# Performance work log

Hardware: AMD Instinct MI355X
Metric: run time of the kernel (lower is better)

## Reference

```python
import jax, jax.numpy as jnp
import numpy as np

E, K = 8, 2            # num_experts, top_k
D, H = 1024, 4096      # d_model, expert_hidden_dim
B, S = 4, 2048         # batch, seq
AUX_W = 0.01


def setup_inputs() -> dict:
    key = jax.random.key(0)
    k0, k1, k2, k3 = jax.random.split(key, 4)
    return {
        "x": jax.random.normal(k0, (B, S, D), jnp.float32),
        "router_w": jax.random.normal(k1, (D, E), jnp.float32) * 0.02,  # normal(0.02) init per MoERouter
        "router_b": jnp.zeros((E,), jnp.float32),
        "w_up": jax.random.normal(k2, (E, D, H), jnp.float32) * (1.0 / np.sqrt(D)),
        "b_up": jnp.zeros((E, H), jnp.float32),
        "w_down": jax.random.normal(k3, (E, H, D), jnp.float32) * (1.0 / np.sqrt(H)),
        "b_down": jnp.zeros((E, D), jnp.float32),
    }


def reference(x, router_w, router_b, w_up, b_up, w_down, b_down):
    # Router
    logits = x @ router_w + router_b                       # (B,S,E)
    router_probs = jax.nn.softmax(logits, axis=-1)         # (B,S,E)
    topk_logits, topk_idx = jax.lax.top_k(logits, K)       # (B,S,K)
    topk_p = jax.nn.softmax(topk_logits, axis=-1)          # (B,S,K)

    # Dense all-expert MLP (matches original: every expert computed on every token)
    h = jax.nn.gelu(jnp.einsum('bsd,edh->bseh', x, w_up) + b_up)   # (B,S,E,H)
    all_out = jnp.einsum('bseh,ehd->bsed', h, w_down) + b_down     # (B,S,E,D)

    # Top-k gather + weighted combine
    sel = jnp.take_along_axis(all_out, topk_idx[..., None], axis=2)  # (B,S,K,D)
    output = jnp.sum(topk_p[..., None] * sel, axis=2)                # (B,S,D)

    # Load-balancing aux loss (Switch/Mixtral formulation)
    counts = jnp.zeros((E,), jnp.float32).at[topk_idx.reshape(-1)].add(1.0)
    fraction = counts / (B * S * K)
    prob_mean = router_probs.mean(axis=(0, 1))
    aux_loss = E * jnp.sum(fraction * prob_mean) * AUX_W
    return output, aux_loss, router_probs
```

## Files before the change

kernel.cpp:

```cpp
#include <hip/hip_runtime.h>
#include <hip/hip_bf16.h>
#include <stdint.h>

constexpr int NT = 8192;
constexpr int NE = 8;
constexpr int ND = 1024;
constexpr int NH = 4096;

constexpr int BM = 256;
constexpr int BN = 256;
constexpr int BK = 32;
constexpr int NBUF = 4;
constexpr int KS_DN = 2;

typedef __attribute__((ext_vector_type(8))) short short8;
typedef __attribute__((ext_vector_type(4))) float f32x4;

constexpr size_t O_XBF  = 0;
constexpr size_t O_WUPT = O_XBF  + (size_t)NT * ND * 2;
constexpr size_t O_WDNT = O_WUPT + (size_t)NE * NH * ND * 2;
constexpr size_t O_HBUF = O_WDNT + (size_t)NE * ND * NH * 2;
constexpr size_t O_STOK = O_HBUF + (size_t)NT * 2 * NH * 2;
constexpr size_t O_SP   = O_STOK + (size_t)NT * 2 * 4;
constexpr size_t O_TKE  = O_SP   + (size_t)NT * 2 * 4;
constexpr size_t O_TKP  = O_TKE  + (size_t)NT * 2 * 4;
constexpr size_t O_CTRL = O_TKP  + (size_t)NT * 2 * 4;
constexpr size_t O_TLUP = O_CTRL + 272;
constexpr size_t O_TLDN = O_TLUP + 160 * 4;

__device__ __forceinline__ void gl_lds16(const void* g, void* l) {
  using GP = char __attribute__((address_space(1))) *;
  using LP = char __attribute__((address_space(3))) *;
  __builtin_amdgcn_global_load_lds((GP)(uintptr_t)g, (LP)(uint32_t)(uintptr_t)l, 16, 0, 0);
}

__device__ __forceinline__ float fast_gelu(float x) {
  float u  = 0.7978845608028654f * (x + 0.044715f * x * x * x);
  float ex = __expf(2.0f * u);
  float th = 1.0f - 2.0f / (ex + 1.0f);
  return 0.5f * x * (1.0f + th);
}

__global__ __launch_bounds__(256) void moe_router(
    const float* __restrict__ x, const float* __restrict__ rw, const float* __restrict__ rb,
    __hip_bfloat16* __restrict__ xbf,
    float* __restrict__ probs_out, int* __restrict__ topk_e, float* __restrict__ topk_p,
    int* __restrict__ cnt_ek, float* __restrict__ probsum)
{
  __shared__ float ps[NE];
  __shared__ int cs[16];
  const int tid = threadIdx.x;
  if (tid < NE) ps[tid] = 0.f;
  if (tid < 16) cs[tid] = 0;
  __syncthreads();
  const int lane = tid & 63, wv = tid >> 6;
  for (int it = 0; it < 8; ++it) {
    const int t = blockIdx.x * 4 + wv + it * 1024;
    const float* xr = x + (size_t)t * ND;
    float acc[NE] = {};
#pragma unroll 4
    for (int j = 0; j < 16; ++j) {
      const int d = j * 64 + lane;
      const float xv = xr[d];
      xbf[(size_t)t * ND + d] = __float2bfloat16(xv);
      const float* w = rw + (size_t)d * NE;
#pragma unroll
      for (int ee = 0; ee < NE; ++ee) acc[ee] += xv * w[ee];
    }
#pragma unroll
    for (int ee = 0; ee < NE; ++ee)
#pragma unroll
      for (int off = 32; off >= 1; off >>= 1)
        acc[ee] += __shfl_down(acc[ee], off, 64);
    if (lane == 0) {
      float lg[NE];
#pragma unroll
      for (int ee = 0; ee < NE; ++ee) lg[ee] = acc[ee] + rb[ee];
      float mx = lg[0];
#pragma unroll
      for (int ee = 1; ee < NE; ++ee) mx = fmaxf(mx, lg[ee]);
      float s = 0.f, pe[NE];
#pragma unroll
      for (int ee = 0; ee < NE; ++ee) { pe[ee] = __expf(lg[ee] - mx); s += pe[ee]; }
      const float inv = 1.f / s;
#pragma unroll
      for (int ee = 0; ee < NE; ++ee) {
        const float pr = pe[ee] * inv;
        probs_out[(size_t)t * NE + ee] = pr;
        atomicAdd(&ps[ee], pr);
      }
      int i1 = 0; float l1 = lg[0];
#pragma unroll
      for (int ee = 1; ee < NE; ++ee) if (lg[ee] > l1) { l1 = lg[ee]; i1 = ee; }
      int i2 = 0; float l2 = -3.0e38f;
#pragma unroll
      for (int ee = 0; ee < NE; ++ee) if (ee != i1 && lg[ee] > l2) { l2 = lg[ee]; i2 = ee; }
      const float e2 = __expf(l2 - l1);
      const float dn = 1.f + e2;
      topk_e[t * 2]     = i1;  topk_e[t * 2 + 1] = i2;
      topk_p[t * 2]     = 1.f / dn;
      topk_p[t * 2 + 1] = e2 / dn;
      atomicAdd(&cs[i1 * 2], 1);
      atomicAdd(&cs[i2 * 2 + 1], 1);
    }
  }
  __syncthreads();
  if (tid < NE) atomicAdd(&probsum[tid], ps[tid]);
  if (tid < 16) atomicAdd(&cnt_ek[tid], cs[tid]);
}

__global__ void moe_finalize(const int* __restrict__ cnt_ek, int* __restrict__ off_ek,
                             const float* __restrict__ probsum, float* __restrict__ aux_out,
                             int* __restrict__ ntiles, int* __restrict__ tl_up,
                             int* __restrict__ tl_dn)
{
  __shared__ int c[16], off[16], uoff[8], ucnt[8], doff[16], dcnt[16];
  const int tid = threadIdx.x;
  if (tid < 16) c[tid] = cnt_ek[tid];
  __syncthreads();
  if (tid == 0) {
    int run = 0;
    for (int i = 0; i < 16; ++i) { off[i] = run; run += c[i]; }
    int ur = 0;
    for (int e = 0; e < NE; ++e) {
      ucnt[e] = (c[2 * e] + c[2 * e + 1] + BM - 1) / BM;
      uoff[e] = ur; ur += ucnt[e];
    }
    ntiles[0] = ur;
    int dr = 0;
    for (int i = 0; i < 16; ++i) {
      dcnt[i] = (c[i] + BM - 1) / BM;
      doff[i] = dr; dr += dcnt[i];
    }
    ntiles[1] = dr;
    float aux = 0.f;
    for (int e = 0; e < NE; ++e) {
      float frac = (float)(c[2 * e] + c[2 * e + 1]) / (float)(NT * 2);
      aux += frac * (probsum[e] / (float)NT);
    }
    aux_out[0] = (float)NE * aux * 0.01f;
  }
  __syncthreads();
  if (tid < 16) off_ek[tid] = off[tid];
  if (tid < 8)
    for (int mb = 0; mb < ucnt[tid]; ++mb) tl_up[uoff[tid] + mb] = (tid << 16) | mb;
  if (tid >= 32 && tid < 48) {
    const int i = tid - 32;
    for (int mb = 0; mb < dcnt[i]; ++mb) tl_dn[doff[i] + mb] = (i << 16) | mb;
  }
}

__global__ __launch_bounds__(256) void moe_scatter(
    const int* __restrict__ topk_e, const float* __restrict__ topk_p,
    const int* __restrict__ off_ek, int* __restrict__ fill_ek,
    int* __restrict__ slot_token, float* __restrict__ slot_p)
{
  __shared__ int lc[16], gb[16], offs[16];
  const int tid = threadIdx.x;
  if (tid < 16) lc[tid] = 0;
  __syncthreads();
  const int t = blockIdx.x * 256 + tid;
  const int id0 = topk_e[t * 2] * 2;
  const int id1 = topk_e[t * 2 + 1] * 2 + 1;
  atomicAdd(&lc[id0], 1);
  atomicAdd(&lc[id1], 1);
  __syncthreads();
  if (tid < 16) {
    gb[tid] = atomicAdd(&fill_ek[tid], lc[tid]);
    offs[tid] = off_ek[tid];
    lc[tid] = 0;
  }
  __syncthreads();
  {
    const int r = atomicAdd(&lc[id0], 1);
    const int slot = offs[id0] + gb[id0] + r;
    slot_token[slot] = t;
    slot_p[slot] = topk_p[t * 2];
  }
  {
    const int r = atomicAdd(&lc[id1], 1);
    const int slot = offs[id1] + gb[id1] + r;
    slot_token[slot] = t;
    slot_p[slot] = topk_p[t * 2 + 1];
  }
}

__global__ __launch_bounds__(256) void moe_transpose_cast(
    const float* __restrict__ in, __hip_bfloat16* __restrict__ outp, int Adim, int Bdim)
{
  __shared__ unsigned short tile[64 * 66];
  const int e = blockIdx.z;
  const int b0 = blockIdx.x * 64, a0 = blockIdx.y * 64;
  const float* ip = in + (size_t)e * Adim * Bdim + (size_t)a0 * Bdim + b0;
  const int c4 = (threadIdx.x & 15) * 4;
  const int r0 = threadIdx.x >> 4;
#pragma unroll
  for (int i = 0; i < 4; ++i) {
    const int r = r0 + i * 16;
    const float4 v = *(const float4*)(ip + (size_t)r * Bdim + c4);
    ushort4 u;
    u.x = __hip_bfloat16_raw(__float2bfloat16(v.x)).x;
    u.y = __hip_bfloat16_raw(__float2bfloat16(v.y)).x;
    u.z = __hip_bfloat16_raw(__float2bfloat16(v.z)).x;
    u.w = __hip_bfloat16_raw(__float2bfloat16(v.w)).x;
    *(ushort4*)&tile[r * 66 + c4] = u;
  }
  __syncthreads();
  unsigned short* op = (unsigned short*)outp + (size_t)e * Bdim * Adim + (size_t)b0 * Adim + a0;
  const int cc  = threadIdx.x >> 2;
  const int rr0 = (threadIdx.x & 3) * 16;
  unsigned short u[16];
#pragma unroll
  for (int i = 0; i < 16; ++i) u[i] = tile[(rr0 + i) * 66 + cc];
  *(short8*)(op + (size_t)cc * Adim + rr0)     = *(short8*)&u[0];
  *(short8*)(op + (size_t)cc * Adim + rr0 + 8) = *(short8*)&u[8];
}


__global__ __launch_bounds__(512, 2) void moe_gemm_up(
    const __hip_bfloat16* __restrict__ xbf,
    const __hip_bfloat16* __restrict__ wupT,
    const float* __restrict__ b_up,
    const int* __restrict__ slot_token,
    const int* __restrict__ cnt_ek, const int* __restrict__ off_ek,
    const int* __restrict__ ntiles, const int* __restrict__ tl_up,
    __hip_bfloat16* __restrict__ hbuf)
{
  if ((int)blockIdx.y >= ntiles[0]) return;
  const int tl = tl_up[blockIdx.y];
  const int e = tl >> 16, mb = tl & 0xffff;
  const int cnt = cnt_ek[2 * e] + cnt_ek[2 * e + 1];
  const int base = off_ek[2 * e];
  const int m0 = mb * BM;
  const int n0 = blockIdx.x * BN;
  const int valid = (cnt - m0 < BM) ? (cnt - m0) : BM;

  __shared__ __align__(16) __hip_bfloat16 As[NBUF][BM * BK];
  __shared__ __align__(16) __hip_bfloat16 Bs[NBUF][BN * BK];

  const int tid = threadIdx.x;
  const int lane = tid & 63, wv = tid >> 6;

  const int r0c = tid >> 2;
  const int k0c = ((tid & 3) ^ ((r0c >> 1) & 3)) * 8;
  const int r1c = r0c + 128;
  const int k1c = ((tid & 3) ^ ((r1c >> 1) & 3)) * 8;
  int srA0 = m0 + r0c; if (srA0 >= cnt) srA0 = cnt - 1;
  int srA1 = m0 + r1c; if (srA1 >= cnt) srA1 = cnt - 1;
  const __hip_bfloat16* gA0 = xbf + (size_t)slot_token[base + srA0] * ND + k0c;
  const __hip_bfloat16* gA1 = xbf + (size_t)slot_token[base + srA1] * ND + k1c;
  const __hip_bfloat16* gB0 = wupT + ((size_t)e * NH + n0 + r0c) * ND + k0c;
  const __hip_bfloat16* gB1 = wupT + ((size_t)e * NH + n0 + r1c) * ND + k1c;

  auto STAGE = [&](int bi, int kk) {
    char* sA = (char*)&As[bi][0] + tid * 16;
    char* sB = (char*)&Bs[bi][0] + tid * 16;
    gl_lds16(gA0 + kk, sA);
    gl_lds16(gA1 + kk, sA + 8192);
    gl_lds16(gB0 + kk, sB);
    gl_lds16(gB1 + kk, sB + 8192);
  };

  const int wm = (wv >> 2) * 128, wn = (wv & 3) * 64;
  const int l15 = lane & 15, q = lane >> 4;
  const int ssw = (q ^ ((l15 >> 1) & 3)) * 16;

  f32x4 acc[8][4] = {};

  auto COMPUTE = [&](int bi) {
    const char* bA = (const char*)&As[bi][0] + (wm + l15) * 64 + ssw;
    const char* bB = (const char*)&Bs[bi][0] + (wn + l15) * 64 + ssw;
    short8 af[8], bfr[4];
#pragma unroll
    for (int i = 0; i < 8; ++i) af[i]  = *(const short8*)(bA + i * 1024);
#pragma unroll
    for (int i = 0; i < 4; ++i) bfr[i] = *(const short8*)(bB + i * 1024);
    __builtin_amdgcn_s_setprio(1);
#pragma unroll
    for (int mt = 0; mt < 8; ++mt)
#pragma unroll
      for (int nt = 0; nt < 4; ++nt)
        acc[mt][nt] = __builtin_amdgcn_mfma_f32_16x16x32_bf16(af[mt], bfr[nt], acc[mt][nt], 0, 0, 0);
    __builtin_amdgcn_s_setprio(0);
  };

  constexpr int KT = ND / BK;
  STAGE(0, 0);
  STAGE(1, BK);
  for (int t = 0; t < KT; ++t) {
    if (t + 2 < KT) {
      STAGE((t + 2) & 3, (t + 2) * BK);
      asm volatile("s_waitcnt vmcnt(8)" ::: "memory");
    } else if (t + 2 == KT) {
      asm volatile("s_waitcnt vmcnt(4)" ::: "memory");
    } else {
      asm volatile("s_waitcnt vmcnt(0)" ::: "memory");
    }
    __builtin_amdgcn_s_barrier();
    __builtin_amdgcn_sched_barrier(0);
    COMPUTE(t & 3);
  }

  float bias[4];
#pragma unroll
  for (int nt = 0; nt < 4; ++nt) bias[nt] = b_up[e * NH + n0 + wn + nt * 16 + l15];
#pragma unroll
  for (int mt = 0; mt < 8; ++mt) {
#pragma unroll
    for (int rr = 0; rr < 4; ++rr) {
      const int row = wm + mt * 16 + q * 4 + rr;
      if (row < valid) {
        const size_t rbase = (size_t)(base + m0 + row) * NH;
#pragma unroll
        for (int nt = 0; nt < 4; ++nt) {
          const int col = n0 + wn + nt * 16 + l15;
          hbuf[rbase + col] = __float2bfloat16(fast_gelu(acc[mt][nt][rr] + bias[nt]));
        }
      }
    }
  }
}

__global__ __launch_bounds__(512, 2) void moe_gemm_down(
    const __hip_bfloat16* __restrict__ hbuf,
    const __hip_bfloat16* __restrict__ wdnT,
    const float* __restrict__ b_down,
    const int* __restrict__ slot_token, const float* __restrict__ slot_p,
    const int* __restrict__ cnt_ek, const int* __restrict__ off_ek,
    const int* __restrict__ ntiles, const int* __restrict__ tl_dn,
    float* __restrict__ out)
{
  if ((int)blockIdx.y >= ntiles[1]) return;
  const int tl = tl_dn[blockIdx.y];
  const int id = tl >> 16, mb = tl & 0xffff;
  const int e = id >> 1;
  const int cnt = cnt_ek[id];
  const int base = off_ek[id];
  const int m0 = mb * BM;
  const int n0 = blockIdx.x * BN;
  const int valid = (cnt - m0 < BM) ? (cnt - m0) : BM;
  const int ks = blockIdx.z;
  const int k_beg = ks * (NH / KS_DN);

  __shared__ __align__(16) __hip_bfloat16 As[NBUF][BM * BK];
  __shared__ __align__(16) __hip_bfloat16 Bs[NBUF][BN * BK];

  const int tid = threadIdx.x;
  const int lane = tid & 63, wv = tid >> 6;

  const int r0c = tid >> 2;
  const int k0c = ((tid & 3) ^ ((r0c >> 1) & 3)) * 8;
  const int r1c = r0c + 128;
  const int k1c = ((tid & 3) ^ ((r1c >> 1) & 3)) * 8;
  int srA0 = m0 + r0c; if (srA0 >= cnt) srA0 = cnt - 1;
  int srA1 = m0 + r1c; if (srA1 >= cnt) srA1 = cnt - 1;
  const __hip_bfloat16* gA0 = hbuf + (size_t)(base + srA0) * NH + k0c;
  const __hip_bfloat16* gA1 = hbuf + (size_t)(base + srA1) * NH + k1c;
  const __hip_bfloat16* gB0 = wdnT + ((size_t)e * ND + n0 + r0c) * NH + k0c;
  const __hip_bfloat16* gB1 = wdnT + ((size_t)e * ND + n0 + r1c) * NH + k1c;

  auto STAGE = [&](int bi, int kk) {
    char* sA = (char*)&As[bi][0] + tid * 16;
    char* sB = (char*)&Bs[bi][0] + tid * 16;
    gl_lds16(gA0 + kk, sA);
    gl_lds16(gA1 + kk, sA + 8192);
    gl_lds16(gB0 + kk, sB);
    gl_lds16(gB1 + kk, sB + 8192);
  };

  const int wm = (wv >> 2) * 128, wn = (wv & 3) * 64;
  const int l15 = lane & 15, q = lane >> 4;
  const int ssw = (q ^ ((l15 >> 1) & 3)) * 16;

  f32x4 acc[8][4] = {};

  auto COMPUTE = [&](int bi) {
    const char* bA = (const char*)&As[bi][0] + (wm + l15) * 64 + ssw;
    const char* bB = (const char*)&Bs[bi][0] + (wn + l15) * 64 + ssw;
    short8 af[8], bfr[4];
#pragma unroll
    for (int i = 0; i < 8; ++i) af[i]  = *(const short8*)(bA + i * 1024);
#pragma unroll
    for (int i = 0; i < 4; ++i) bfr[i] = *(const short8*)(bB + i * 1024);
    __builtin_amdgcn_s_setprio(1);
#pragma unroll
    for (int mt = 0; mt < 8; ++mt)
#pragma unroll
      for (int nt = 0; nt < 4; ++nt)
        acc[mt][nt] = __builtin_amdgcn_mfma_f32_16x16x32_bf16(af[mt], bfr[nt], acc[mt][nt], 0, 0, 0);
    __builtin_amdgcn_s_setprio(0);
  };

  constexpr int KT = (NH / KS_DN) / BK;
  STAGE(0, k_beg);
  STAGE(1, k_beg + BK);
  for (int t = 0; t < KT; ++t) {
    if (t + 2 < KT) {
      STAGE((t + 2) & 3, k_beg + (t + 2) * BK);
      asm volatile("s_waitcnt vmcnt(8)" ::: "memory");
    } else if (t + 2 == KT) {
      asm volatile("s_waitcnt vmcnt(4)" ::: "memory");
    } else {
      asm volatile("s_waitcnt vmcnt(0)" ::: "memory");
    }
    __builtin_amdgcn_s_barrier();
    __builtin_amdgcn_sched_barrier(0);
    COMPUTE(t & 3);
  }

  float bias[4];
#pragma unroll
  for (int nt = 0; nt < 4; ++nt)
    bias[nt] = (ks == 0) ? b_down[e * ND + n0 + wn + nt * 16 + l15] : 0.f;
#pragma unroll
  for (int mt = 0; mt < 8; ++mt) {
#pragma unroll
    for (int rr = 0; rr < 4; ++rr) {
      const int row = wm + mt * 16 + q * 4 + rr;
      if (row < valid) {
        const int slot = base + m0 + row;
        const int tok = slot_token[slot];
        const float p = slot_p[slot];
        const size_t obase = (size_t)tok * ND;
#pragma unroll
        for (int nt = 0; nt < 4; ++nt) {
          const int col = n0 + wn + nt * 16 + l15;
          atomicAdd(&out[obase + col], (acc[mt][nt][rr] + bias[nt]) * p);
        }
      }
    }
  }
}

extern "C" void kernel_launch(void* const* d_in, const int* in_sizes, int n_in,
                              void* d_out, int out_size, void* d_ws, size_t ws_size,
                              hipStream_t stream) {
  (void)in_sizes; (void)n_in; (void)out_size; (void)ws_size;
  const float* x   = (const float*)d_in[0];
  const float* rw  = (const float*)d_in[1];
  const float* rb  = (const float*)d_in[2];
  const float* wup = (const float*)d_in[3];
  const float* bup = (const float*)d_in[4];
  const float* wdn = (const float*)d_in[5];
  const float* bdn = (const float*)d_in[6];
  float* out = (float*)d_out;

  char* ws = (char*)d_ws;
  __hip_bfloat16* xbf  = (__hip_bfloat16*)(ws + O_XBF);
  __hip_bfloat16* wupT = (__hip_bfloat16*)(ws + O_WUPT);
  __hip_bfloat16* wdnT = (__hip_bfloat16*)(ws + O_WDNT);
  __hip_bfloat16* hbuf = (__hip_bfloat16*)(ws + O_HBUF);
  int*   slot_token = (int*)(ws + O_STOK);
  float* slot_p     = (float*)(ws + O_SP);
  int*   topk_e     = (int*)(ws + O_TKE);
  float* topk_p     = (float*)(ws + O_TKP);
  int*   cnt_ek  = (int*)(ws + O_CTRL);
  int*   fill_ek = (int*)(ws + O_CTRL + 64);
  float* probsum = (float*)(ws + O_CTRL + 128);
  int*   off_ek  = (int*)(ws + O_CTRL + 192);
  int*   ntiles  = (int*)(ws + O_CTRL + 256);
  int*   tl_up   = (int*)(ws + O_TLUP);
  int*   tl_dn   = (int*)(ws + O_TLDN);

  hipMemsetAsync(ws + O_CTRL, 0, 272, stream);
  hipMemsetAsync(out, 0, (size_t)NT * ND * sizeof(float), stream);

  moe_transpose_cast<<<dim3(NH / 64, ND / 64, NE), 256, 0, stream>>>(wup, wupT, ND, NH);
  moe_transpose_cast<<<dim3(ND / 64, NH / 64, NE), 256, 0, stream>>>(wdn, wdnT, NH, ND);

  moe_router<<<256, 256, 0, stream>>>(x, rw, rb, xbf, out + (size_t)NT * ND + 1,
                                      topk_e, topk_p, cnt_ek, probsum);
  moe_finalize<<<1, 64, 0, stream>>>(cnt_ek, off_ek, probsum, out + (size_t)NT * ND,
                                     ntiles, tl_up, tl_dn);
  moe_scatter<<<NT / 256, 256, 0, stream>>>(topk_e, topk_p, off_ek, fill_ek, slot_token, slot_p);

  moe_gemm_up<<<dim3(NH / BN, 72, 1), 512, 0, stream>>>(
      xbf, wupT, bup, slot_token, cnt_ek, off_ek, ntiles, tl_up, hbuf);
  moe_gemm_down<<<dim3(ND / BN, 80, KS_DN), 512, 0, stream>>>(
      hbuf, wdnT, bdn, slot_token, slot_p, cnt_ek, off_ek, ntiles, tl_dn, out);
}
```

Before: 868.7 us.

## Restructure GEMM main loops into double-K ping-pong with interleaved LDS reads and MFMAs

```diff
diff --git a/kernel.cpp b/kernel.cpp
--- a/kernel.cpp
+++ b/kernel.cpp
@@ -10,11 +10,12 @@
 constexpr int BM = 256;
 constexpr int BN = 256;
 constexpr int BK = 32;
-constexpr int NBUF = 4;
 constexpr int KS_DN = 2;
 
 typedef __attribute__((ext_vector_type(8))) short short8;
 typedef __attribute__((ext_vector_type(4))) float f32x4;
+
+#define SB() __builtin_amdgcn_sched_barrier(0)
 
 constexpr size_t O_XBF  = 0;
 constexpr size_t O_WUPT = O_XBF  + (size_t)NT * ND * 2;
@@ -216,6 +217,16 @@
   *(short8*)(op + (size_t)cc * Adim + rr0 + 8) = *(short8*)&u[8];
 }
 
+
+#define MFMA8(aX, aY, bA, mtX, mtY)                                            \
+  __builtin_amdgcn_s_setprio(1);                                               \
+  _Pragma("unroll")                                                            \
+  for (int nt = 0; nt < 4; ++nt)                                               \
+    acc[mtX][nt] = __builtin_amdgcn_mfma_f32_16x16x32_bf16(aX, bA[nt], acc[mtX][nt], 0, 0, 0); \
+  _Pragma("unroll")                                                            \
+  for (int nt = 0; nt < 4; ++nt)                                               \
+    acc[mtY][nt] = __builtin_amdgcn_mfma_f32_16x16x32_bf16(aY, bA[nt], acc[mtY][nt], 0, 0, 0); \
+  __builtin_amdgcn_s_setprio(0);
 
 __global__ __launch_bounds__(512, 2) void moe_gemm_up(
     const __hip_bfloat16* __restrict__ xbf,
@@ -235,8 +246,8 @@
   const int n0 = blockIdx.x * BN;
   const int valid = (cnt - m0 < BM) ? (cnt - m0) : BM;
 
-  __shared__ __align__(16) __hip_bfloat16 As[NBUF][BM * BK];
-  __shared__ __align__(16) __hip_bfloat16 Bs[NBUF][BN * BK];
+  __shared__ __align__(16) __hip_bfloat16 As[4][BM * BK];
+  __shared__ __align__(16) __hip_bfloat16 Bs[4][BN * BK];
 
   const int tid = threadIdx.x;
   const int lane = tid & 63, wv = tid >> 6;
@@ -252,53 +263,72 @@
   const __hip_bfloat16* gB0 = wupT + ((size_t)e * NH + n0 + r0c) * ND + k0c;
   const __hip_bfloat16* gB1 = wupT + ((size_t)e * NH + n0 + r1c) * ND + k1c;
 
-  auto STAGE = [&](int bi, int kk) {
-    char* sA = (char*)&As[bi][0] + tid * 16;
-    char* sB = (char*)&Bs[bi][0] + tid * 16;
-    gl_lds16(gA0 + kk, sA);
-    gl_lds16(gA1 + kk, sA + 8192);
-    gl_lds16(gB0 + kk, sB);
-    gl_lds16(gB1 + kk, sB + 8192);
-  };
+  char* sA0 = (char*)&As[0][0] + tid * 16;  char* sB0 = (char*)&Bs[0][0] + tid * 16;
+  char* sA1 = (char*)&As[1][0] + tid * 16;  char* sB1 = (char*)&Bs[1][0] + tid * 16;
+  char* sA2 = (char*)&As[2][0] + tid * 16;  char* sB2 = (char*)&Bs[2][0] + tid * 16;
+  char* sA3 = (char*)&As[3][0] + tid * 16;  char* sB3 = (char*)&Bs[3][0] + tid * 16;
 
   const int wm = (wv >> 2) * 128, wn = (wv & 3) * 64;
   const int l15 = lane & 15, q = lane >> 4;
   const int ssw = (q ^ ((l15 >> 1) & 3)) * 16;
+  const char* rA0 = (const char*)&As[0][0] + (wm + l15) * 64 + ssw;
+  const char* rA1 = (const char*)&As[1][0] + (wm + l15) * 64 + ssw;
+  const char* rA2 = (const char*)&As[2][0] + (wm + l15) * 64 + ssw;
+  const char* rA3 = (const char*)&As[3][0] + (wm + l15) * 64 + ssw;
+  const char* rB0 = (const char*)&Bs[0][0] + (wn + l15) * 64 + ssw;
+  const char* rB1 = (const char*)&Bs[1][0] + (wn + l15) * 64 + ssw;
+  const char* rB2 = (const char*)&Bs[2][0] + (wn + l15) * 64 + ssw;
+  const char* rB3 = (const char*)&Bs[3][0] + (wn + l15) * 64 + ssw;
 
   f32x4 acc[8][4] = {};
 
-  auto COMPUTE = [&](int bi) {
-    const char* bA = (const char*)&As[bi][0] + (wm + l15) * 64 + ssw;
-    const char* bB = (const char*)&Bs[bi][0] + (wn + l15) * 64 + ssw;
-    short8 af[8], bfr[4];
-#pragma unroll
-    for (int i = 0; i < 8; ++i) af[i]  = *(const short8*)(bA + i * 1024);
-#pragma unroll
-    for (int i = 0; i < 4; ++i) bfr[i] = *(const short8*)(bB + i * 1024);
-    __builtin_amdgcn_s_setprio(1);
-#pragma unroll
-    for (int mt = 0; mt < 8; ++mt)
-#pragma unroll
-      for (int nt = 0; nt < 4; ++nt)
-        acc[mt][nt] = __builtin_amdgcn_mfma_f32_16x16x32_bf16(af[mt], bfr[nt], acc[mt][nt], 0, 0, 0);
-    __builtin_amdgcn_s_setprio(0);
+  auto STAGEP = [&](char* xA0, char* xB0, char* xA1, char* xB1, int kk) {
+    gl_lds16(gA0 + kk, xA0);        gl_lds16(gA1 + kk, xA0 + 8192);
+    gl_lds16(gB0 + kk, xB0);        gl_lds16(gB1 + kk, xB0 + 8192);
+    gl_lds16(gA0 + kk + BK, xA1);   gl_lds16(gA1 + kk + BK, xA1 + 8192);
+    gl_lds16(gB0 + kk + BK, xB1);   gl_lds16(gB1 + kk + BK, xB1 + 8192);
   };
 
-  constexpr int KT = ND / BK;
-  STAGE(0, 0);
-  STAGE(1, BK);
-  for (int t = 0; t < KT; ++t) {
-    if (t + 2 < KT) {
-      STAGE((t + 2) & 3, (t + 2) * BK);
-      asm volatile("s_waitcnt vmcnt(8)" ::: "memory");
-    } else if (t + 2 == KT) {
-      asm volatile("s_waitcnt vmcnt(4)" ::: "memory");
-    } else {
-      asm volatile("s_waitcnt vmcnt(0)" ::: "memory");
-    }
+  auto KSTEP = [&](const char* pA0, const char* pB0, const char* pA1, const char* pB1,
+                   char* xA0, char* xB0, char* xA1, char* xB1, int knext, bool do_stage) {
+    asm volatile("s_waitcnt vmcnt(0)" ::: "memory");
     __builtin_amdgcn_s_barrier();
-    __builtin_amdgcn_sched_barrier(0);
-    COMPUTE(t & 3);
+    if (do_stage) STAGEP(xA0, xB0, xA1, xB1, knext);
+    short8 b0[4], b1[4];
+    short8 a00, a01, a02, a03, a04, a05, a06, a07;
+    short8 a10, a11, a12, a13, a14, a15, a16, a17;
+#pragma unroll
+    for (int i = 0; i < 4; ++i) b0[i] = *(const short8*)(pB0 + i * 1024);
+    a00 = *(const short8*)(pA0);
+    a01 = *(const short8*)(pA0 + 1024);
+    SB();
+    a02 = *(const short8*)(pA0 + 2048); a03 = *(const short8*)(pA0 + 3072); SB();
+    MFMA8(a00, a01, b0, 0, 1); SB();
+    a04 = *(const short8*)(pA0 + 4096); a05 = *(const short8*)(pA0 + 5120); SB();
+    MFMA8(a02, a03, b0, 2, 3); SB();
+    a06 = *(const short8*)(pA0 + 6144); a07 = *(const short8*)(pA0 + 7168); SB();
+    MFMA8(a04, a05, b0, 4, 5); SB();
+#pragma unroll
+    for (int i = 0; i < 4; ++i) b1[i] = *(const short8*)(pB1 + i * 1024);
+    a10 = *(const short8*)(pA1);
+    a11 = *(const short8*)(pA1 + 1024);
+    SB();
+    MFMA8(a06, a07, b0, 6, 7); SB();
+    a12 = *(const short8*)(pA1 + 2048); a13 = *(const short8*)(pA1 + 3072); SB();
+    MFMA8(a10, a11, b1, 0, 1); SB();
+    a14 = *(const short8*)(pA1 + 4096); a15 = *(const short8*)(pA1 + 5120); SB();
+    MFMA8(a12, a13, b1, 2, 3); SB();
+    a16 = *(const short8*)(pA1 + 6144); a17 = *(const short8*)(pA1 + 7168); SB();
+    MFMA8(a14, a15, b1, 4, 5); SB();
+    MFMA8(a16, a17, b1, 6, 7);
+  };
+
+  constexpr int NK = ND / 64;
+  STAGEP(sA0, sB0, sA1, sB1, 0);
+#pragma unroll 1
+  for (int j = 0; j < NK; j += 2) {
+    KSTEP(rA0, rB0, rA1, rB1, sA2, sB2, sA3, sB3, (j + 1) * 64, j + 1 < NK);
+    KSTEP(rA2, rB2, rA3, rB3, sA0, sB0, sA1, sB1, (j + 2) * 64, j + 2 < NK);
   }
 
   float bias[4];
@@ -342,8 +372,8 @@
   const int ks = blockIdx.z;
   const int k_beg = ks * (NH / KS_DN);
 
-  __shared__ __align__(16) __hip_bfloat16 As[NBUF][BM * BK];
-  __shared__ __align__(16) __hip_bfloat16 Bs[NBUF][BN * BK];
+  __shared__ __align__(16) __hip_bfloat16 As[4][BM * BK];
+  __shared__ __align__(16) __hip_bfloat16 Bs[4][BN * BK];
 
   const int tid = threadIdx.x;
   const int lane = tid & 63, wv = tid >> 6;
@@ -359,53 +389,72 @@
   const __hip_bfloat16* gB0 = wdnT + ((size_t)e * ND + n0 + r0c) * NH + k0c;
   const __hip_bfloat16* gB1 = wdnT + ((size_t)e * ND + n0 + r1c) * NH + k1c;
 
-  auto STAGE = [&](int bi, int kk) {
-    char* sA = (char*)&As[bi][0] + tid * 16;
-    char* sB = (char*)&Bs[bi][0] + tid * 16;
-    gl_lds16(gA0 + kk, sA);
-    gl_lds16(gA1 + kk, sA + 8192);
-    gl_lds16(gB0 + kk, sB);
-    gl_lds16(gB1 + kk, sB + 8192);
-  };
+  char* sA0 = (char*)&As[0][0] + tid * 16;  char* sB0 = (char*)&Bs[0][0] + tid * 16;
+  char* sA1 = (char*)&As[1][0] + tid * 16;  char* sB1 = (char*)&Bs[1][0] + tid * 16;
+  char* sA2 = (char*)&As[2][0] + tid * 16;  char* sB2 = (char*)&Bs[2][0] + tid * 16;
+  char* sA3 = (char*)&As[3][0] + tid * 16;  char* sB3 = (char*)&Bs[3][0] + tid * 16;
 
   const int wm = (wv >> 2) * 128, wn = (wv & 3) * 64;
   const int l15 = lane & 15, q = lane >> 4;
   const int ssw = (q ^ ((l15 >> 1) & 3)) * 16;
+  const char* rA0 = (const char*)&As[0][0] + (wm + l15) * 64 + ssw;
+  const char* rA1 = (const char*)&As[1][0] + (wm + l15) * 64 + ssw;
+  const char* rA2 = (const char*)&As[2][0] + (wm + l15) * 64 + ssw;
+  const char* rA3 = (const char*)&As[3][0] + (wm + l15) * 64 + ssw;
+  const char* rB0 = (const char*)&Bs[0][0] + (wn + l15) * 64 + ssw;
+  const char* rB1 = (const char*)&Bs[1][0] + (wn + l15) * 64 + ssw;
+  const char* rB2 = (const char*)&Bs[2][0] + (wn + l15) * 64 + ssw;
+  const char* rB3 = (const char*)&Bs[3][0] + (wn + l15) * 64 + ssw;
 
   f32x4 acc[8][4] = {};
 
-  auto COMPUTE = [&](int bi) {
-    const char* bA = (const char*)&As[bi][0] + (wm + l15) * 64 + ssw;
-    const char* bB = (const char*)&Bs[bi][0] + (wn + l15) * 64 + ssw;
-    short8 af[8], bfr[4];
-#pragma unroll
-    for (int i = 0; i < 8; ++i) af[i]  = *(const short8*)(bA + i * 1024);
-#pragma unroll
-    for (int i = 0; i < 4; ++i) bfr[i] = *(const short8*)(bB + i * 1024);
-    __builtin_amdgcn_s_setprio(1);
-#pragma unroll
-    for (int mt = 0; mt < 8; ++mt)
-#pragma unroll
-      for (int nt = 0; nt < 4; ++nt)
-        acc[mt][nt] = __builtin_amdgcn_mfma_f32_16x16x32_bf16(af[mt], bfr[nt], acc[mt][nt], 0, 0, 0);
-    __builtin_amdgcn_s_setprio(0);
+  auto STAGEP = [&](char* xA0, char* xB0, char* xA1, char* xB1, int kk) {
+    gl_lds16(gA0 + kk, xA0);        gl_lds16(gA1 + kk, xA0 + 8192);
+    gl_lds16(gB0 + kk, xB0);        gl_lds16(gB1 + kk, xB0 + 8192);
+    gl_lds16(gA0 + kk + BK, xA1);   gl_lds16(gA1 + kk + BK, xA1 + 8192);
+    gl_lds16(gB0 + kk + BK, xB1);   gl_lds16(gB1 + kk + BK, xB1 + 8192);
   };
 
-  constexpr int KT = (NH / KS_DN) / BK;
-  STAGE(0, k_beg);
-  STAGE(1, k_beg + BK);
-  for (int t = 0; t < KT; ++t) {
-    if (t + 2 < KT) {
-      STAGE((t + 2) & 3, k_beg + (t + 2) * BK);
-      asm volatile("s_waitcnt vmcnt(8)" ::: "memory");
-    } else if (t + 2 == KT) {
-      asm volatile("s_waitcnt vmcnt(4)" ::: "memory");
-    } else {
-      asm volatile("s_waitcnt vmcnt(0)" ::: "memory");
-    }
+  auto KSTEP = [&](const char* pA0, const char* pB0, const char* pA1, const char* pB1,
+                   char* xA0, char* xB0, char* xA1, char* xB1, int knext, bool do_stage) {
+    asm volatile("s_waitcnt vmcnt(0)" ::: "memory");
     __builtin_amdgcn_s_barrier();
-    __builtin_amdgcn_sched_barrier(0);
-    COMPUTE(t & 3);
+    if (do_stage) STAGEP(xA0, xB0, xA1, xB1, knext);
+    short8 b0[4], b1[4];
+    short8 a00, a01, a02, a03, a04, a05, a06, a07;
+    short8 a10, a11, a12, a13, a14, a15, a16, a17;
+#pragma unroll
+    for (int i = 0; i < 4; ++i) b0[i] = *(const short8*)(pB0 + i * 1024);
+    a00 = *(const short8*)(pA0);
+    a01 = *(const short8*)(pA0 + 1024);
+    SB();
+    a02 = *(const short8*)(pA0 + 2048); a03 = *(const short8*)(pA0 + 3072); SB();
+    MFMA8(a00, a01, b0, 0, 1); SB();
+    a04 = *(const short8*)(pA0 + 4096); a05 = *(const short8*)(pA0 + 5120); SB();
+    MFMA8(a02, a03, b0, 2, 3); SB();
+    a06 = *(const short8*)(pA0 + 6144); a07 = *(const short8*)(pA0 + 7168); SB();
+    MFMA8(a04, a05, b0, 4, 5); SB();
+#pragma unroll
+    for (int i = 0; i < 4; ++i) b1[i] = *(const short8*)(pB1 + i * 1024);
+    a10 = *(const short8*)(pA1);
+    a11 = *(const short8*)(pA1 + 1024);
+    SB();
+    MFMA8(a06, a07, b0, 6, 7); SB();
+    a12 = *(const short8*)(pA1 + 2048); a13 = *(const short8*)(pA1 + 3072); SB();
+    MFMA8(a10, a11, b1, 0, 1); SB();
+    a14 = *(const short8*)(pA1 + 4096); a15 = *(const short8*)(pA1 + 5120); SB();
+    MFMA8(a12, a13, b1, 2, 3); SB();
+    a16 = *(const short8*)(pA1 + 6144); a17 = *(const short8*)(pA1 + 7168); SB();
+    MFMA8(a14, a15, b1, 4, 5); SB();
+    MFMA8(a16, a17, b1, 6, 7);
+  };
+
+  constexpr int NK = (NH / KS_DN) / 64;
+  STAGEP(sA0, sB0, sA1, sB1, k_beg);
+#pragma unroll 1
+  for (int j = 0; j < NK; j += 2) {
+    KSTEP(rA0, rB0, rA1, rB1, sA2, sB2, sA3, sB3, k_beg + (j + 1) * 64, j + 1 < NK);
+    KSTEP(rA2, rB2, rA3, rB3, sA0, sB0, sA1, sB1, k_beg + (j + 2) * 64, j + 2 < NK);
   }
 
   float bias[4];
```

Result: no change. 883.4 us (+1.7%).
